# Kernel optimization log

Measured on AMD Instinct MI355X. Metric: run time of the kernel, lower is better.

Reference implementation:

```python
import jax, jax.numpy as jnp
import numpy as np

T, B = 512, 2048
IN, E, H = 12, 15, 20


def setup_inputs() -> dict:
    key = jax.random.key(0)
    ks = jax.random.split(key, 9)
    def rnd(k, shape, scale):
        return jax.random.normal(k, shape, dtype=jnp.float32) * scale
    return {
        "marker_detections": rnd(ks[0], (T, B, IN), 1.0),
        "W_emb": rnd(ks[1], (E, IN), 1.0 / np.sqrt(IN)),
        "b_emb": rnd(ks[2], (E,), 0.1),
        "W_ih": rnd(ks[3], (4 * H, E), 1.0 / np.sqrt(H)),
        "b_ih": rnd(ks[4], (4 * H,), 0.1),
        "W_hh": rnd(ks[5], (4 * H, H), 1.0 / np.sqrt(H)),
        "b_hh": rnd(ks[6], (4 * H,), 0.1),
        "W_out": rnd(ks[7], (3, H), 1.0 / np.sqrt(H)),
        "b_out": rnd(ks[8], (3,), 0.1),
    }


def _lstm(x_gates, W_hh, b_hh, hidden_dim):
    # x_gates: (T, B, 4H) precomputed input projections (PyTorch gate order i,f,g,o)
    Bsz = x_gates.shape[1]
    h0 = jnp.zeros((Bsz, hidden_dim), x_gates.dtype)
    c0 = jnp.zeros((Bsz, hidden_dim), x_gates.dtype)

    def step(carry, xg):
        h, c = carry
        gates = xg + h @ W_hh.T + b_hh  # (B, 4H)
        i, f, g, o = jnp.split(gates, 4, axis=-1)
        i = jax.nn.sigmoid(i)
        f = jax.nn.sigmoid(f)
        g = jnp.tanh(g)
        o = jax.nn.sigmoid(o)
        c = f * c + i * g
        h = o * jnp.tanh(c)
        return (h, c), h

    _, hs = jax.lax.scan(step, (h0, c0), x_gates)
    return hs  # (T, B, H)


def reference(marker_detections, W_emb, b_emb, W_ih, b_ih, W_hh, b_hh, W_out, b_out):
    # embeddings: (T, B, E)
    emb = marker_detections @ W_emb.T + b_emb
    # precompute input-to-gate projections for all timesteps: (T, B, 4H)
    x_gates = emb @ W_ih.T + b_ih
    hs = _lstm(x_gates, W_hh, b_hh, H)  # (T, B, H)
    pos_space = hs @ W_out.T + b_out  # (T, B, 3)
    return pos_space
```

## Files before the change

### kernel.cpp

```cpp
#include <hip/hip_runtime.h>

#define T_STEPS 512
#define BATCH   2048
#define IN_F    12
#define E_F     15
#define H_F     20
#define G4      80
#define TC      32
#define NCHUNK  (T_STEPS / TC)

typedef float v2f __attribute__((ext_vector_type(2)));

#define OFF_MD   0
#define OFF_H    768
#define OFF_WC   (768 + 48)
#define OFF_BC   (OFF_WC + 960)
#define OFF_RAW  (OFF_BC + 80)
#define RAW_WEMB 0
#define RAW_WIH  180
#define RAW_BEMB 1380
#define RAW_BIH  1395
#define RAW_BHH  1475
#define SMEM_FLOATS (OFF_RAW + 1555)

__device__ __forceinline__ float fsig(float x) {
    float e = __builtin_amdgcn_exp2f(x * -1.442695040888963f);
    return __builtin_amdgcn_rcpf(1.0f + e);
}
__device__ __forceinline__ float ftanh(float x) {
    float e = __builtin_amdgcn_exp2f(x * -2.885390081777927f);
    return fmaf(2.0f, __builtin_amdgcn_rcpf(1.0f + e), -1.0f);
}
__device__ __forceinline__ v2f pkfma(v2f a, v2f b, v2f c) {
    return __builtin_elementwise_fma(a, b, c);
}

__global__ __launch_bounds__(64, 1) void lstm_tracker_kernel(
    const float* __restrict__ md,
    const float* __restrict__ W_emb, const float* __restrict__ b_emb,
    const float* __restrict__ W_ih,  const float* __restrict__ b_ih,
    const float* __restrict__ W_hh,  const float* __restrict__ b_hh,
    const float* __restrict__ W_out, const float* __restrict__ b_out,
    float* __restrict__ out)
{
    __shared__ __align__(16) float smem[SMEM_FLOATS];
    const int lane = threadIdx.x;
    const int bl   = lane >> 5;
    const int j    = lane & 31;
    const int jj   = (j < H_F) ? j : 0;
    const int b    = blockIdx.x * 2 + bl;

    float* raw = smem + OFF_RAW;
    for (int i = lane; i < E_F * IN_F; i += 64) raw[RAW_WEMB + i] = W_emb[i];
    for (int i = lane; i < G4 * E_F;  i += 64) raw[RAW_WIH  + i] = W_ih[i];
    if (lane < E_F) raw[RAW_BEMB + lane] = b_emb[lane];
    for (int g = lane; g < G4; g += 64) raw[RAW_BIH + g] = b_ih[g];
    for (int g = lane; g < G4; g += 64) raw[RAW_BHH + g] = b_hh[g];
    __syncthreads();

    for (int idx = lane; idx < G4 * IN_F; idx += 64) {
        int g = idx / IN_F, c = idx - g * IN_F;
        float s = 0.f;
        #pragma unroll
        for (int e = 0; e < E_F; ++e)
            s += raw[RAW_WIH + g * E_F + e] * raw[RAW_WEMB + e * IN_F + c];
        smem[OFF_WC + idx] = s;
    }
    for (int g = lane; g < G4; g += 64) {
        float s = raw[RAW_BIH + g] + raw[RAW_BHH + g];
        #pragma unroll
        for (int e = 0; e < E_F; ++e)
            s += raw[RAW_WIH + g * E_F + e] * raw[RAW_BEMB + e];
        smem[OFF_BC + g] = s;
    }
    __syncthreads();

    v2f wcI[6], wcF[6], wcG[6], wcO[6];
    #pragma unroll
    for (int k = 0; k < 6; ++k) {
        wcI[k] = *(const v2f*)(smem + OFF_WC + (jj           ) * IN_F + 2 * k);
        wcF[k] = *(const v2f*)(smem + OFF_WC + (jj +     H_F ) * IN_F + 2 * k);
        wcG[k] = *(const v2f*)(smem + OFF_WC + (jj + 2 * H_F ) * IN_F + 2 * k);
        wcO[k] = *(const v2f*)(smem + OFF_WC + (jj + 3 * H_F ) * IN_F + 2 * k);
    }
    const float bcI = smem[OFF_BC + jj];
    const float bcF = smem[OFF_BC + jj + H_F];
    const float bcG = smem[OFF_BC + jj + 2 * H_F];
    const float bcO = smem[OFF_BC + jj + 3 * H_F];

    v2f whI[10], whF[10], whG[10], whO[10];
    #pragma unroll
    for (int k = 0; k < 10; ++k) {
        whI[k] = *(const v2f*)(W_hh + (jj           ) * H_F + 2 * k);
        whF[k] = *(const v2f*)(W_hh + (jj +     H_F ) * H_F + 2 * k);
        whG[k] = *(const v2f*)(W_hh + (jj + 2 * H_F ) * H_F + 2 * k);
        whO[k] = *(const v2f*)(W_hh + (jj + 3 * H_F ) * H_F + 2 * k);
    }
    const int rr = (j < 3) ? j : 0;
    v2f wo[10];
    #pragma unroll
    for (int k = 0; k < 10; ++k) wo[k] = *(const v2f*)(W_out + rr * H_F + 2 * k);
    const float bo = b_out[rr];

    v2f h2[10];
    #pragma unroll
    for (int k = 0; k < 10; ++k) h2[k] = (v2f){0.f, 0.f};
    float cc = 0.f;

    #pragma unroll 1
    for (int ch = 0; ch < NCHUNK; ++ch) {
        __syncthreads();

        for (int idx = lane; idx < TC * 6; idx += 64) {
            int tt = idx / 6, w = idx - tt * 6;
            const float* src = md + ((size_t)(ch * TC + tt) * BATCH + (size_t)blockIdx.x * 2) * IN_F + w * 4;
            *(float4*)(smem + OFF_MD + tt * 24 + w * 4) = *(const float4*)src;
        }
        __syncthreads();

        const float4* mr0 = (const float4*)(smem + OFF_MD + bl * IN_F);
        float4 m0 = mr0[0], m1 = mr0[1], m2 = mr0[2];

        #pragma unroll 1
        for (int tt = 0; tt < TC; ++tt) {
            v2f mm0 = {m0.x, m0.y}, mm1 = {m0.z, m0.w}, mm2 = {m1.x, m1.y};
            v2f mm3 = {m1.z, m1.w}, mm4 = {m2.x, m2.y}, mm5 = {m2.z, m2.w};
            v2f aI = pkfma(wcI[0], mm0, pkfma(wcI[1], mm1, pkfma(wcI[2], mm2,
                     pkfma(wcI[3], mm3, pkfma(wcI[4], mm4, wcI[5] * mm5)))));
            v2f aF = pkfma(wcF[0], mm0, pkfma(wcF[1], mm1, pkfma(wcF[2], mm2,
                     pkfma(wcF[3], mm3, pkfma(wcF[4], mm4, wcF[5] * mm5)))));
            v2f aG = pkfma(wcG[0], mm0, pkfma(wcG[1], mm1, pkfma(wcG[2], mm2,
                     pkfma(wcG[3], mm3, pkfma(wcG[4], mm4, wcG[5] * mm5)))));
            v2f aO = pkfma(wcO[0], mm0, pkfma(wcO[1], mm1, pkfma(wcO[2], mm2,
                     pkfma(wcO[3], mm3, pkfma(wcO[4], mm4, wcO[5] * mm5)))));
            float ai = bcI + aI.x + aI.y;
            float af = bcF + aF.x + aF.y;
            float ag = bcG + aG.x + aG.y;
            float ao = bcO + aO.x + aO.y;

            if (tt + 1 < TC) {
                const float4* mn = (const float4*)(smem + OFF_MD + (tt + 1) * 24 + bl * IN_F);
                m0 = mn[0]; m1 = mn[1]; m2 = mn[2];
            }

            const int st = ch * TC + tt;
            v2f pa = pkfma(wo[0], h2[0], pkfma(wo[1], h2[1], pkfma(wo[2], h2[2],
                     pkfma(wo[3], h2[3], pkfma(wo[4], h2[4], pkfma(wo[5], h2[5],
                     pkfma(wo[6], h2[6], pkfma(wo[7], h2[7], pkfma(wo[8], h2[8],
                     wo[9] * h2[9])))))))));
            if (j < 3 && st > 0)
                out[((size_t)(st - 1) * BATCH + b) * 3 + j] = pa.x + pa.y + bo;

            v2f rI = pkfma(whI[0], h2[0], pkfma(whI[1], h2[1], pkfma(whI[2], h2[2],
                     pkfma(whI[3], h2[3], pkfma(whI[4], h2[4], pkfma(whI[5], h2[5],
                     pkfma(whI[6], h2[6], pkfma(whI[7], h2[7], pkfma(whI[8], h2[8],
                     whI[9] * h2[9])))))))));
            v2f rF = pkfma(whF[0], h2[0], pkfma(whF[1], h2[1], pkfma(whF[2], h2[2],
                     pkfma(whF[3], h2[3], pkfma(whF[4], h2[4], pkfma(whF[5], h2[5],
                     pkfma(whF[6], h2[6], pkfma(whF[7], h2[7], pkfma(whF[8], h2[8],
                     whF[9] * h2[9])))))))));
            v2f rG = pkfma(whG[0], h2[0], pkfma(whG[1], h2[1], pkfma(whG[2], h2[2],
                     pkfma(whG[3], h2[3], pkfma(whG[4], h2[4], pkfma(whG[5], h2[5],
                     pkfma(whG[6], h2[6], pkfma(whG[7], h2[7], pkfma(whG[8], h2[8],
                     whG[9] * h2[9])))))))));
            v2f rO = pkfma(whO[0], h2[0], pkfma(whO[1], h2[1], pkfma(whO[2], h2[2],
                     pkfma(whO[3], h2[3], pkfma(whO[4], h2[4], pkfma(whO[5], h2[5],
                     pkfma(whO[6], h2[6], pkfma(whO[7], h2[7], pkfma(whO[8], h2[8],
                     whO[9] * h2[9])))))))));
            ai += rI.x + rI.y;
            af += rF.x + rF.y;
            ag += rG.x + rG.y;
            ao += rO.x + rO.y;

            float gi = fsig(ai);
            float gf = fsig(af);
            float gt = ftanh(ag);
            float go = fsig(ao);
            cc = fmaf(gf, cc, gi * gt);
            float hown = go * ftanh(cc);

            if (j < H_F) smem[OFF_H + bl * 24 + jj] = hown;
            const float4* hr = (const float4*)(smem + OFF_H + bl * 24);
            float4 h0 = hr[0], h1 = hr[1], hx = hr[2], h3 = hr[3], h4 = hr[4];
            h2[0] = (v2f){h0.x, h0.y}; h2[1] = (v2f){h0.z, h0.w};
            h2[2] = (v2f){h1.x, h1.y}; h2[3] = (v2f){h1.z, h1.w};
            h2[4] = (v2f){hx.x, hx.y}; h2[5] = (v2f){hx.z, hx.w};
            h2[6] = (v2f){h3.x, h3.y}; h2[7] = (v2f){h3.z, h3.w};
            h2[8] = (v2f){h4.x, h4.y}; h2[9] = (v2f){h4.z, h4.w};
        }
    }

    v2f pa = pkfma(wo[0], h2[0], pkfma(wo[1], h2[1], pkfma(wo[2], h2[2],
             pkfma(wo[3], h2[3], pkfma(wo[4], h2[4], pkfma(wo[5], h2[5],
             pkfma(wo[6], h2[6], pkfma(wo[7], h2[7], pkfma(wo[8], h2[8],
             wo[9] * h2[9])))))))));
    if (j < 3)
        out[((size_t)(T_STEPS - 1) * BATCH + b) * 3 + j] = pa.x + pa.y + bo;
}

extern "C" void kernel_launch(void* const* d_in, const int* in_sizes, int n_in,
                              void* d_out, int out_size, void* d_ws, size_t ws_size,
                              hipStream_t stream) {
    const float* md    = (const float*)d_in[0];
    const float* W_emb = (const float*)d_in[1];
    const float* b_emb = (const float*)d_in[2];
    const float* W_ih  = (const float*)d_in[3];
    const float* b_ih  = (const float*)d_in[4];
    const float* W_hh  = (const float*)d_in[5];
    const float* b_hh  = (const float*)d_in[6];
    const float* W_out = (const float*)d_in[7];
    const float* b_out = (const float*)d_in[8];
    float* out = (float*)d_out;

    hipLaunchKernelGGL(lstm_tracker_kernel, dim3(BATCH / 2), dim3(64), 0, stream,
                       md, W_emb, b_emb, W_ih, b_ih, W_hh, b_hh, W_out, b_out, out);
}
```

Before: 302.3 us.

## Map one batch element per wave, drop barriers, pin weights in registers

Each 64-thread block now handles one batch element instead of two, so the grid doubles and a block is a single wavefront. With one wave per block the __syncthreads calls are removed, relying on in-wave lockstep for LDS visibility. The marker chunk grows to 64 timesteps, launch bounds allow two blocks per CU, and inline-asm pins keep weights in VGPRs. In exchange, 44 of 64 lanes sit idle per wave instead of 24, and dropping barriers assumes wavefront-synchronous LDS ordering.

New measurement: 440.2 us. 45.6% more time.

```diff
diff --git a/kernel.cpp b/kernel.cpp
--- a/kernel.cpp
+++ b/kernel.cpp
@@ -6,14 +6,14 @@
 #define E_F     15
 #define H_F     20
 #define G4      80
-#define TC      32
+#define TC      64
 #define NCHUNK  (T_STEPS / TC)
 
 typedef float v2f __attribute__((ext_vector_type(2)));
 
 #define OFF_MD   0
 #define OFF_H    768
-#define OFF_WC   (768 + 48)
+#define OFF_WC   (768 + 24)
 #define OFF_BC   (OFF_WC + 960)
 #define OFF_RAW  (OFF_BC + 80)
 #define RAW_WEMB 0
@@ -23,6 +23,8 @@
 #define RAW_BHH  1475
 #define SMEM_FLOATS (OFF_RAW + 1555)
 
+#define PIN(x) asm volatile("" : "+v"(x))
+
 __device__ __forceinline__ float fsig(float x) {
     float e = __builtin_amdgcn_exp2f(x * -1.442695040888963f);
     return __builtin_amdgcn_rcpf(1.0f + e);
@@ -35,7 +37,7 @@
     return __builtin_elementwise_fma(a, b, c);
 }
 
-__global__ __launch_bounds__(64, 1) void lstm_tracker_kernel(
+__global__ __launch_bounds__(64, 2) void lstm_tracker_kernel(
     const float* __restrict__ md,
     const float* __restrict__ W_emb, const float* __restrict__ b_emb,
     const float* __restrict__ W_ih,  const float* __restrict__ b_ih,
@@ -45,10 +47,9 @@
 {
     __shared__ __align__(16) float smem[SMEM_FLOATS];
     const int lane = threadIdx.x;
-    const int bl   = lane >> 5;
-    const int j    = lane & 31;
+    const int j    = lane;
     const int jj   = (j < H_F) ? j : 0;
-    const int b    = blockIdx.x * 2 + bl;
+    const int b    = blockIdx.x;
 
     float* raw = smem + OFF_RAW;
     for (int i = lane; i < E_F * IN_F; i += 64) raw[RAW_WEMB + i] = W_emb[i];
@@ -56,7 +57,6 @@
     if (lane < E_F) raw[RAW_BEMB + lane] = b_emb[lane];
     for (int g = lane; g < G4; g += 64) raw[RAW_BIH + g] = b_ih[g];
     for (int g = lane; g < G4; g += 64) raw[RAW_BHH + g] = b_hh[g];
-    __syncthreads();
 
     for (int idx = lane; idx < G4 * IN_F; idx += 64) {
         int g = idx / IN_F, c = idx - g * IN_F;
@@ -73,7 +73,6 @@
             s += raw[RAW_WIH + g * E_F + e] * raw[RAW_BEMB + e];
         smem[OFF_BC + g] = s;
     }
-    __syncthreads();
 
     v2f wcI[6], wcF[6], wcG[6], wcO[6];
     #pragma unroll
@@ -82,11 +81,13 @@
         wcF[k] = *(const v2f*)(smem + OFF_WC + (jj +     H_F ) * IN_F + 2 * k);
         wcG[k] = *(const v2f*)(smem + OFF_WC + (jj + 2 * H_F ) * IN_F + 2 * k);
         wcO[k] = *(const v2f*)(smem + OFF_WC + (jj + 3 * H_F ) * IN_F + 2 * k);
-    }
-    const float bcI = smem[OFF_BC + jj];
-    const float bcF = smem[OFF_BC + jj + H_F];
-    const float bcG = smem[OFF_BC + jj + 2 * H_F];
-    const float bcO = smem[OFF_BC + jj + 3 * H_F];
+        PIN(wcI[k]); PIN(wcF[k]); PIN(wcG[k]); PIN(wcO[k]);
+    }
+    float bcI = smem[OFF_BC + jj];
+    float bcF = smem[OFF_BC + jj + H_F];
+    float bcG = smem[OFF_BC + jj + 2 * H_F];
+    float bcO = smem[OFF_BC + jj + 3 * H_F];
+    PIN(bcI); PIN(bcF); PIN(bcG); PIN(bcO);
 
     v2f whI[10], whF[10], whG[10], whO[10];
     #pragma unroll
@@ -95,12 +96,17 @@
         whF[k] = *(const v2f*)(W_hh + (jj +     H_F ) * H_F + 2 * k);
         whG[k] = *(const v2f*)(W_hh + (jj + 2 * H_F ) * H_F + 2 * k);
         whO[k] = *(const v2f*)(W_hh + (jj + 3 * H_F ) * H_F + 2 * k);
+        PIN(whI[k]); PIN(whF[k]); PIN(whG[k]); PIN(whO[k]);
     }
     const int rr = (j < 3) ? j : 0;
     v2f wo[10];
     #pragma unroll
-    for (int k = 0; k < 10; ++k) wo[k] = *(const v2f*)(W_out + rr * H_F + 2 * k);
-    const float bo = b_out[rr];
+    for (int k = 0; k < 10; ++k) {
+        wo[k] = *(const v2f*)(W_out + rr * H_F + 2 * k);
+        PIN(wo[k]);
+    }
+    float bo = b_out[rr];
+    PIN(bo);
 
     v2f h2[10];
     #pragma unroll
@@ -109,16 +115,13 @@
 
     #pragma unroll 1
     for (int ch = 0; ch < NCHUNK; ++ch) {
-        __syncthreads();
-
-        for (int idx = lane; idx < TC * 6; idx += 64) {
-            int tt = idx / 6, w = idx - tt * 6;
-            const float* src = md + ((size_t)(ch * TC + tt) * BATCH + (size_t)blockIdx.x * 2) * IN_F + w * 4;
-            *(float4*)(smem + OFF_MD + tt * 24 + w * 4) = *(const float4*)src;
+        for (int idx = lane; idx < TC * 3; idx += 64) {
+            int tt = idx / 3, w = idx - tt * 3;
+            const float* src = md + ((size_t)(ch * TC + tt) * BATCH + b) * IN_F + w * 4;
+            *(float4*)(smem + OFF_MD + tt * IN_F + w * 4) = *(const float4*)src;
         }
-        __syncthreads();
-
-        const float4* mr0 = (const float4*)(smem + OFF_MD + bl * IN_F);
+
+        const float4* mr0 = (const float4*)(smem + OFF_MD);
         float4 m0 = mr0[0], m1 = mr0[1], m2 = mr0[2];
 
         #pragma unroll 1
@@ -139,7 +142,7 @@
             float ao = bcO + aO.x + aO.y;
 
             if (tt + 1 < TC) {
-                const float4* mn = (const float4*)(smem + OFF_MD + (tt + 1) * 24 + bl * IN_F);
+                const float4* mn = (const float4*)(smem + OFF_MD + (tt + 1) * IN_F);
                 m0 = mn[0]; m1 = mn[1]; m2 = mn[2];
             }
 
@@ -179,8 +182,8 @@
             cc = fmaf(gf, cc, gi * gt);
             float hown = go * ftanh(cc);
 
-            if (j < H_F) smem[OFF_H + bl * 24 + jj] = hown;
-            const float4* hr = (const float4*)(smem + OFF_H + bl * 24);
+            if (j < H_F) smem[OFF_H + j] = hown;
+            const float4* hr = (const float4*)(smem + OFF_H);
             float4 h0 = hr[0], h1 = hr[1], hx = hr[2], h3 = hr[3], h4 = hr[4];
             h2[0] = (v2f){h0.x, h0.y}; h2[1] = (v2f){h0.z, h0.w};
             h2[2] = (v2f){h1.x, h1.y}; h2[3] = (v2f){h1.z, h1.w};
@@ -212,6 +215,6 @@
     const float* b_out = (const float*)d_in[8];
     float* out = (float*)d_out;
 
-    hipLaunchKernelGGL(lstm_tracker_kernel, dim3(BATCH / 2), dim3(64), 0, stream,
+    hipLaunchKernelGGL(lstm_tracker_kernel, dim3(BATCH), dim3(64), 0, stream,
                        md, W_emb, b_emb, W_ih, b_ih, W_hh, b_hh, W_out, b_out, out);
 }
```
